# Optimization experiments

Measured on AMD Instinct MI355X. Metric: run time of the kernel, lower is better.

The kernel has to match this reference:

```python
import jax, jax.numpy as jnp
import numpy as np

N = 100000   # nodes
E = 1600000  # edges
G = 64       # graphs
D_IN, D_H, D_OUT = 128, 128, 64


def setup_inputs() -> dict:
    key = jax.random.key(0)
    ks = jax.random.split(key, 24)
    def p(k, shape, fan_in):
        return jax.random.normal(k, shape, jnp.float32) / np.sqrt(fan_in)
    inp = {
        "x": jax.random.normal(ks[0], (N, D_IN), jnp.float32),
        "W0r": p(ks[1], (D_H, D_IN), D_IN), "W0i": p(ks[2], (D_H, D_IN), D_IN),
        "b0r": jnp.zeros((D_H,), jnp.float32), "b0i": jnp.zeros((D_H,), jnp.float32),
        "M0r": p(ks[3], (D_H, D_H), D_H), "M0i": p(ks[4], (D_H, D_H), D_H),
        "c0r": jnp.zeros((D_H,), jnp.float32), "c0i": jnp.zeros((D_H,), jnp.float32),
        "t0r": jnp.float32(1.0), "t0i": jnp.zeros((1,), jnp.float32),
        "W1r": p(ks[5], (D_OUT, D_H), D_H), "W1i": p(ks[6], (D_OUT, D_H), D_H),
        "b1r": jnp.zeros((D_OUT,), jnp.float32), "b1i": jnp.zeros((D_OUT,), jnp.float32),
        "M1r": p(ks[7], (D_OUT, D_OUT), D_OUT), "M1i": p(ks[8], (D_OUT, D_OUT), D_OUT),
        "c1r": jnp.zeros((D_OUT,), jnp.float32), "c1i": jnp.zeros((D_OUT,), jnp.float32),
        "t1r": jnp.float32(1.0), "t1i": jnp.zeros((1,), jnp.float32),
        "edge_index": jax.random.randint(ks[9], (2, E), 0, N, dtype=jnp.int64),
        "batch": jnp.sort(jax.random.randint(ks[10], (N,), 0, G, dtype=jnp.int64)),
    }
    return inp


def _complex_relu(z):
    return jax.nn.relu(z.real) + 1j * jax.nn.relu(z.imag)


def _layer(x, Wr, Wi, br, bi, Mr, Mi, cr, ci, tr, ti, src, dst):
    # complex linear: x @ W^T + b
    W = Wr + 1j * Wi
    x = x @ W.T + (br + 1j * bi)
    x = _complex_relu(x)
    t = tr + 1j * ti  # complex time param, shape [1]
    time_factor = jnp.exp(-1j * t)
    # msg_lin applied at node level (linear commutes with gather), then gather at src
    m = (x @ (Mr + 1j * Mi).T + (cr + 1j * ci)) * time_factor
    aggr = jax.ops.segment_sum(m[src], dst, num_segments=N)
    ef = jnp.exp(-1j * t * 0.5)
    return x * ef + aggr * (1 - ef)


def reference(x, W0r, W0i, b0r, b0i, M0r, M0i, c0r, c0i, t0r, t0i,
              W1r, W1i, b1r, b1i, M1r, M1i, c1r, c1i, t1r, t1i,
              edge_index, batch):
    src, dst = edge_index[0], edge_index[1]
    xc = x.astype(jnp.complex64)
    xc = _layer(xc, W0r, W0i, b0r, b0i, M0r, M0i, c0r, c0i, t0r, t0i, src, dst)
    xc = _layer(xc, W1r, W1i, b1r, b1i, M1r, M1i, c1r, c1i, t1r, t1i, src, dst)
    a = jnp.abs(xc)  # [N, D_OUT] float32
    sums = jax.ops.segment_sum(a, batch, num_segments=G)
    counts = jax.ops.segment_sum(jnp.ones((N,), a.dtype), batch, num_segments=G)
    mean = sums / jnp.clip(counts, 1.0)[:, None]
    return jax.nn.log_softmax(mean, axis=1)
```

## Files before the change

### kernel.cpp

```cpp
#include <hip/hip_runtime.h>

typedef __attribute__((ext_vector_type(8))) short bf16x8;
typedef __attribute__((ext_vector_type(4))) float f32x4;

__device__ __forceinline__ float b2f(unsigned short u) {
    return __uint_as_float(((unsigned int)u) << 16);
}
__device__ __forceinline__ unsigned short f2b(float f) {
    unsigned int u = __float_as_uint(f);
    unsigned int r = (u + 0x7FFFu + ((u >> 16) & 1u)) >> 16;
    return (unsigned short)r;
}

#define EDGE_CHUNK 2048

__global__ __launch_bounds__(256) void prep_build_kernel(
    const float* __restrict__ W0r, const float* __restrict__ W0i, unsigned short* __restrict__ V0,
    const float* __restrict__ M0r, const float* __restrict__ M0i, unsigned short* __restrict__ VM0,
    const float* __restrict__ W1r, const float* __restrict__ W1i, unsigned short* __restrict__ V1,
    const float* __restrict__ M1r, const float* __restrict__ M1i, unsigned short* __restrict__ VM1,
    const int* __restrict__ src, const int* __restrict__ dst,
    int* __restrict__ deg, int* __restrict__ csr, int E, int N)
{
    int b = blockIdx.x;
    if (b < 64) {
        int idx = b * 256 + threadIdx.x;
        int j = idx >> 7, k = idx & 127;
        V0[(size_t)(2 * j) * 128 + k]     = f2b(W0r[idx]);
        V0[(size_t)(2 * j + 1) * 128 + k] = f2b(W0i[idx]);
    } else if (b < 128) {
        int idx = (b - 64) * 256 + threadIdx.x;
        int j = idx >> 7, kk = idx & 127;
        float wr = M0r[idx], wi = M0i[idx];
        unsigned short* r0 = VM0 + (size_t)(2 * j) * 256 + 2 * kk;
        unsigned short* r1 = VM0 + (size_t)(2 * j + 1) * 256 + 2 * kk;
        r0[0] = f2b(wr);  r0[1] = f2b(-wi);
        r1[0] = f2b(wi);  r1[1] = f2b(wr);
    } else if (b < 160) {
        int idx = (b - 128) * 256 + threadIdx.x;
        int j = idx >> 7, kk = idx & 127;
        float wr = W1r[idx], wi = W1i[idx];
        unsigned short* r0 = V1 + (size_t)(2 * j) * 256 + 2 * kk;
        unsigned short* r1 = V1 + (size_t)(2 * j + 1) * 256 + 2 * kk;
        r0[0] = f2b(wr);  r0[1] = f2b(-wi);
        r1[0] = f2b(wi);  r1[1] = f2b(wr);
    } else if (b < 176) {
        int idx = (b - 160) * 256 + threadIdx.x;
        int j = idx >> 6, kk = idx & 63;
        float wr = M1r[idx], wi = M1i[idx];
        unsigned short* r0 = VM1 + (size_t)(2 * j) * 128 + 2 * kk;
        unsigned short* r1 = VM1 + (size_t)(2 * j + 1) * 128 + 2 * kk;
        r0[0] = f2b(wr);  r0[1] = f2b(-wi);
        r1[0] = f2b(wi);  r1[1] = f2b(wr);
    } else {
        int vb = b - 176;
        int x  = vb & 7;
        int c  = vb >> 3;
        int lo = (int)((long long)N * x / 8);
        int hi = (int)((long long)N * (x + 1) / 8);
        int base = c * EDGE_CHUNK;
        int end  = min(base + EDGE_CHUNK, E);
        for (int e = base + threadIdx.x; e < end; e += 256) {
            int d = __builtin_nontemporal_load(dst + e);
            if (d >= lo && d < hi) {
                int s = __builtin_nontemporal_load(src + e);
                if ((unsigned)s < (unsigned)N) {
                    int pos = atomicAdd(&deg[d], 1);
                    if (pos < 64) csr[((size_t)d << 6) + pos] = s;
                }
            }
        }
    }
}

template<int Kr, int TWOJ, int AMODE, bool CRELU, bool MIX, bool WF8>
__global__ __launch_bounds__(256) void mfma_cgemm_kernel(
    const void* __restrict__ Xv,
    const unsigned short* __restrict__ Vg,
    const float* __restrict__ br, const float* __restrict__ bi,
    const float* __restrict__ trp, const float* __restrict__ tip,
    const unsigned short* __restrict__ Hin, const int* __restrict__ degp,
    unsigned short* __restrict__ Out, unsigned char* __restrict__ Of8,
    int nNodes)
{
    constexpr int TILES  = TWOJ / 16;
    constexpr int FT     = TILES / 4;
    constexpr int CHUNKS = Kr / 32;
    constexpr int VROW   = 40;
    static_assert(TILES % 4 == 0, "TILES % 4");

    __shared__ __align__(16) unsigned short sV[TWOJ * VROW];
    __shared__ __align__(16) unsigned short sA[64 * VROW];

    const int tid  = threadIdx.x;
    const int w    = tid >> 6;
    const int lane = tid & 63;
    const int l15  = lane & 15;
    const int q    = lane >> 4;
    const int n0   = blockIdx.x * 64;
    const int tq   = w * FT;

    f32x4 acc[FT][4];
    #pragma unroll
    for (int t = 0; t < FT; ++t)
        #pragma unroll
        for (int nt = 0; nt < 4; ++nt) acc[t][nt] = (f32x4){0.f, 0.f, 0.f, 0.f};

    for (int kc = 0; kc < CHUNKS; ++kc) {
        #pragma unroll
        for (int it = 0; it < TWOJ / 64; ++it) {
            int idx = it * 256 + tid;
            int row = idx >> 2;
            int seg = idx & 3;
            *(uint4*)(sV + row * VROW + seg * 8) =
                *(const uint4*)(Vg + (size_t)row * Kr + kc * 32 + seg * 8);
        }
        if constexpr (AMODE == 0) {
            const float* X = (const float*)Xv;
            #pragma unroll
            for (int it = 0; it < 2; ++it) {
                int idx = it * 256 + tid;
                int nl = idx >> 3;
                int cg = idx & 7;
                int n  = n0 + nl;
                f32x4 v = (f32x4){0.f, 0.f, 0.f, 0.f};
                if (n < nNodes)
                    v = __builtin_nontemporal_load(
                        (const f32x4*)(X + (size_t)n * Kr + kc * 32 + cg * 4));
                *(ushort4*)(sA + nl * VROW + cg * 4) =
                    make_ushort4(f2b(v[0]), f2b(v[1]), f2b(v[2]), f2b(v[3]));
            }
        } else {
            const unsigned short* X = (const unsigned short*)Xv;
            int nl  = tid >> 2;
            int seg = tid & 3;
            int n   = n0 + nl;
            uint4 v = make_uint4(0, 0, 0, 0);
            if (n < nNodes)
                v = *(const uint4*)(X + (size_t)n * Kr + kc * 32 + seg * 8);
            *(uint4*)(sA + nl * VROW + seg * 8) = v;
        }
        __syncthreads();

        bf16x8 bfrag[4];
        #pragma unroll
        for (int nt = 0; nt < 4; ++nt)
            bfrag[nt] = *(const bf16x8*)(sA + (nt * 16 + l15) * VROW + q * 8);
        #pragma unroll
        for (int t = 0; t < FT; ++t) {
            bf16x8 afrag = *(const bf16x8*)(sV + ((tq + t) * 16 + l15) * VROW + q * 8);
            #pragma unroll
            for (int nt = 0; nt < 4; ++nt)
                acc[t][nt] = __builtin_amdgcn_mfma_f32_16x16x32_bf16(
                    afrag, bfrag[nt], acc[t][nt], 0, 0, 0);
        }
        __syncthreads();
    }

    float Fr = 1.f, Fi = 0.f, efr = 1.f, efi = 0.f;
    if constexpr (MIX) {
        float tr = trp[0], ti = tip[0];
        float er  = expf(ti);
        float tfr =  er * cosf(tr);
        float tfi = -er * sinf(tr);
        float eh  = expf(0.5f * ti);
        efr =  eh * cosf(0.5f * tr);
        efi = -eh * sinf(0.5f * tr);
        float omr = 1.f - efr, omi = -efi;
        Fr = tfr * omr - tfi * omi;
        Fi = tfr * omi + tfi * omr;
    }
    #pragma unroll
    for (int nt = 0; nt < 4; ++nt) {
        int n = n0 + nt * 16 + l15;
        if (n >= nNodes) continue;
        float dg = 0.f;
        if constexpr (MIX) dg = (float)degp[n];
        #pragma unroll
        for (int t = 0; t < FT; ++t) {
            int f0 = (tq + t) * 16 + q * 4;
            int j0 = f0 >> 1;
            float re0, im0, re1, im1;
            if constexpr (MIX) {
                float ar0 = acc[t][nt][0] + dg * br[j0];
                float ai0 = acc[t][nt][1] + dg * bi[j0];
                float ar1 = acc[t][nt][2] + dg * br[j0 + 1];
                float ai1 = acc[t][nt][3] + dg * bi[j0 + 1];
                re0 = ar0 * Fr - ai0 * Fi;  im0 = ar0 * Fi + ai0 * Fr;
                re1 = ar1 * Fr - ai1 * Fi;  im1 = ar1 * Fi + ai1 * Fr;
                ushort4 hu = *(const ushort4*)(Hin + (size_t)n * TWOJ + f0);
                float hr0 = b2f(hu.x), hi0 = b2f(hu.y), hr1 = b2f(hu.z), hi1 = b2f(hu.w);
                re0 += hr0 * efr - hi0 * efi;  im0 += hr0 * efi + hi0 * efr;
                re1 += hr1 * efr - hi1 * efi;  im1 += hr1 * efi + hi1 * efr;
            } else {
                re0 = acc[t][nt][0] + br[j0];
                im0 = acc[t][nt][1] + bi[j0];
                re1 = acc[t][nt][2] + br[j0 + 1];
                im1 = acc[t][nt][3] + bi[j0 + 1];
                if constexpr (CRELU) {
                    re0 = fmaxf(re0, 0.f); im0 = fmaxf(im0, 0.f);
                    re1 = fmaxf(re1, 0.f); im1 = fmaxf(im1, 0.f);
                }
            }
            *(ushort4*)(Out + (size_t)n * TWOJ + f0) =
                make_ushort4(f2b(re0), f2b(im0), f2b(re1), f2b(im1));
            if constexpr (WF8) {
                int pk = 0;
                pk = __builtin_amdgcn_cvt_pk_fp8_f32(re0, im0, pk, false);
                pk = __builtin_amdgcn_cvt_pk_fp8_f32(re1, im1, pk, true);
                *(int*)(Of8 + (size_t)n * TWOJ + f0) = pk;
            }
        }
    }
}

template<int ROWE>
__global__ __launch_bounds__(256) void gather_f8_kernel(
    const unsigned char* __restrict__ h8, unsigned short* __restrict__ agg,
    const int* __restrict__ deg, const int* __restrict__ csr, int N)
{
    constexpr int LPR = ROWE / 16;
    constexpr int NPW = 64 / LPR;
    const int tid  = threadIdx.x;
    const int lane = tid & 63;
    const int wid  = (blockIdx.x * 256 + tid) >> 6;
    if (wid * NPW >= N) return;
    const int g    = lane / LPR;
    const int sub  = lane % LPR;
    const int nid  = wid * NPW + g;
    const bool nv  = nid < N;
    int dg = 0;
    if (nv) dg = min(deg[nid], 64);

    uint4 cq0 = make_uint4(0, 0, 0, 0), cq1 = make_uint4(0, 0, 0, 0);
    if (nv) {
        const uint4* cp = (const uint4*)csr + ((size_t)nid << 4);
        cq0 = cp[sub];
        if constexpr (LPR == 8) cq1 = cp[8 + sub];
    }

    int mx = dg;
    mx = max(mx, __shfl_xor(mx, 32, 64));
    mx = max(mx, __shfl_xor(mx, 16, 64));
    if constexpr (LPR == 8) mx = max(mx, __shfl_xor(mx, 8, 64));

    float a[16];
    #pragma unroll
    for (int k = 0; k < 16; ++k) a[k] = 0.f;

    const unsigned char* hp = h8 + sub * 16;
    const int gb = g * LPR;

    #define CVT16(uu)                                                          \
        {                                                                      \
            auto p0 = __builtin_amdgcn_cvt_pk_f32_fp8((uu).x, false);          \
            a[0] += p0[0];   a[1] += p0[1];                                    \
            auto p1 = __builtin_amdgcn_cvt_pk_f32_fp8((uu).x, true);           \
            a[2] += p1[0];   a[3] += p1[1];                                    \
            auto p2 = __builtin_amdgcn_cvt_pk_f32_fp8((uu).y, false);          \
            a[4] += p2[0];   a[5] += p2[1];                                    \
            auto p3 = __builtin_amdgcn_cvt_pk_f32_fp8((uu).y, true);           \
            a[6] += p3[0];   a[7] += p3[1];                                    \
            auto p4 = __builtin_amdgcn_cvt_pk_f32_fp8((uu).z, false);          \
            a[8] += p4[0];   a[9] += p4[1];                                    \
            auto p5 = __builtin_amdgcn_cvt_pk_f32_fp8((uu).z, true);           \
            a[10] += p5[0];  a[11] += p5[1];                                   \
            auto p6 = __builtin_amdgcn_cvt_pk_f32_fp8((uu).w, false);          \
            a[12] += p6[0];  a[13] += p6[1];                                   \
            auto p7 = __builtin_amdgcn_cvt_pk_f32_fp8((uu).w, true);           \
            a[14] += p7[0];  a[15] += p7[1];                                   \
        }

    for (int e = 0; e < mx; e += 8) {
        uint4 cq = cq0;
        if constexpr (LPR == 8) { if (e & 32) cq = cq1; }
        const int o0 = gb + ((e & (4 * LPR - 1)) >> 2);
        const int o1 = o0 + 1;
        int s0 = __shfl((int)cq.x, o0, 64);
        int s1 = __shfl((int)cq.y, o0, 64);
        int s2 = __shfl((int)cq.z, o0, 64);
        int s3 = __shfl((int)cq.w, o0, 64);
        int s4 = __shfl((int)cq.x, o1, 64);
        int s5 = __shfl((int)cq.y, o1, 64);
        int s6 = __shfl((int)cq.z, o1, 64);
        int s7 = __shfl((int)cq.w, o1, 64);
        uint4 u0 = make_uint4(0,0,0,0), u1 = make_uint4(0,0,0,0);
        uint4 u2 = make_uint4(0,0,0,0), u3 = make_uint4(0,0,0,0);
        uint4 u4 = make_uint4(0,0,0,0), u5 = make_uint4(0,0,0,0);
        uint4 u6 = make_uint4(0,0,0,0), u7 = make_uint4(0,0,0,0);
        if (e + 0 < dg) u0 = *(const uint4*)(hp + (size_t)(unsigned)s0 * ROWE);
        if (e + 1 < dg) u1 = *(const uint4*)(hp + (size_t)(unsigned)s1 * ROWE);
        if (e + 2 < dg) u2 = *(const uint4*)(hp + (size_t)(unsigned)s2 * ROWE);
        if (e + 3 < dg) u3 = *(const uint4*)(hp + (size_t)(unsigned)s3 * ROWE);
        if (e + 4 < dg) u4 = *(const uint4*)(hp + (size_t)(unsigned)s4 * ROWE);
        if (e + 5 < dg) u5 = *(const uint4*)(hp + (size_t)(unsigned)s5 * ROWE);
        if (e + 6 < dg) u6 = *(const uint4*)(hp + (size_t)(unsigned)s6 * ROWE);
        if (e + 7 < dg) u7 = *(const uint4*)(hp + (size_t)(unsigned)s7 * ROWE);
        CVT16(u0) CVT16(u1) CVT16(u2) CVT16(u3)
        CVT16(u4) CVT16(u5) CVT16(u6) CVT16(u7)
    }
    #undef CVT16

    if (nv) {
        unsigned short* op = agg + (size_t)nid * ROWE + sub * 16;
        *(ushort4*)(op)      = make_ushort4(f2b(a[0]),  f2b(a[1]),  f2b(a[2]),  f2b(a[3]));
        *(ushort4*)(op + 4)  = make_ushort4(f2b(a[4]),  f2b(a[5]),  f2b(a[6]),  f2b(a[7]));
        *(ushort4*)(op + 8)  = make_ushort4(f2b(a[8]),  f2b(a[9]),  f2b(a[10]), f2b(a[11]));
        *(ushort4*)(op + 12) = make_ushort4(f2b(a[12]), f2b(a[13]), f2b(a[14]), f2b(a[15]));
    }
}

__global__ __launch_bounds__(256) void abs_reduce_kernel(
    const unsigned short* __restrict__ z, const int* __restrict__ batch,
    float* __restrict__ sums, int N)
{
    constexpr int NPW = 16;
    int wid  = (blockIdx.x * 256 + threadIdx.x) >> 6;
    int lane = threadIdx.x & 63;
    int nBeg = wid * NPW;
    if (nBeg >= N) return;
    int nEnd = min(nBeg + NPW, N);

    float acc = 0.f;
    int cur_g = batch[nBeg];
    for (int n = nBeg; n < nEnd; ++n) {
        unsigned int u = *(const unsigned int*)(z + ((size_t)n << 7) + (lane << 1));
        float zr = b2f((unsigned short)(u & 0xffffu));
        float zi = b2f((unsigned short)(u >> 16));
        float a = sqrtf(zr * zr + zi * zi);
        int g = batch[n];
        if (g != cur_g) {
            if ((unsigned)cur_g < 64u) unsafeAtomicAdd(&sums[cur_g * 64 + lane], acc);
            acc = 0.f;
            cur_g = g;
        }
        acc += a;
    }
    if ((unsigned)cur_g < 64u) unsafeAtomicAdd(&sums[cur_g * 64 + lane], acc);
}

__global__ __launch_bounds__(64) void finalize_kernel(
    const float* __restrict__ sums, const int* __restrict__ batch,
    float* __restrict__ out, int N)
{
    int g = blockIdx.x, d = threadIdx.x;
    __shared__ int cnt_s;
    if (d == 0) {
        int lo = 0, hi = N;
        while (lo < hi) { int mid = (lo + hi) >> 1; if (batch[mid] < g) lo = mid + 1; else hi = mid; }
        int lo2 = lo, hi2 = N;
        while (lo2 < hi2) { int mid = (lo2 + hi2) >> 1; if (batch[mid] < g + 1) lo2 = mid + 1; else hi2 = mid; }
        cnt_s = lo2 - lo;
    }
    __syncthreads();
    float c = fmaxf((float)cnt_s, 1.0f);
    float m = sums[g * 64 + d] / c;
    float mx = m;
    #pragma unroll
    for (int o = 32; o > 0; o >>= 1) mx = fmaxf(mx, __shfl_xor(mx, o, 64));
    float e = expf(m - mx);
    float s = e;
    #pragma unroll
    for (int o = 32; o > 0; o >>= 1) s += __shfl_xor(s, o, 64);
    out[g * 64 + d] = m - mx - logf(s);
}

extern "C" void kernel_launch(void* const* d_in, const int* in_sizes, int n_in,
                              void* d_out, int out_size, void* d_ws, size_t ws_size,
                              hipStream_t stream)
{
    const float* x   = (const float*)d_in[0];
    const float* W0r = (const float*)d_in[1];
    const float* W0i = (const float*)d_in[2];
    const float* b0r = (const float*)d_in[3];
    const float* b0i = (const float*)d_in[4];
    const float* M0r = (const float*)d_in[5];
    const float* M0i = (const float*)d_in[6];
    const float* c0r = (const float*)d_in[7];
    const float* c0i = (const float*)d_in[8];
    const float* t0r = (const float*)d_in[9];
    const float* t0i = (const float*)d_in[10];
    const float* W1r = (const float*)d_in[11];
    const float* W1i = (const float*)d_in[12];
    const float* b1r = (const float*)d_in[13];
    const float* b1i = (const float*)d_in[14];
    const float* M1r = (const float*)d_in[15];
    const float* M1i = (const float*)d_in[16];
    const float* c1r = (const float*)d_in[17];
    const float* c1i = (const float*)d_in[18];
    const float* t1r = (const float*)d_in[19];
    const float* t1i = (const float*)d_in[20];
    const int* edge  = (const int*)d_in[21];
    const int* batch = (const int*)d_in[22];

    const int N = in_sizes[0] / 128;
    const int E = in_sizes[21] / 2;
    const int* src = edge;
    const int* dst = edge + E;

    unsigned short* h0   = (unsigned short*)d_ws;
    unsigned short* aggA = h0 + (size_t)N * 256;
    unsigned short* h1   = aggA + (size_t)N * 256;
    unsigned short* aggB = h1 + (size_t)N * 128;
    int*   deg  = (int*)(aggB + (size_t)N * 128);
    int*   csr  = deg + N;
    float* sums = (float*)(csr + (size_t)N * 64);
    unsigned short* V0  = (unsigned short*)(sums + 4096);
    unsigned short* VM0 = V0  + 256 * 128;
    unsigned short* V1  = VM0 + 256 * 256;
    unsigned short* VM1 = V1  + 128 * 256;
    unsigned char* hf8 = (unsigned char*)(VM1 + 128 * 128);

    const int gemmGrid  = (N + 63) / 64;
    const int buildGrid = ((E + EDGE_CHUNK - 1) / EDGE_CHUNK) * 8;
    const int pbGrid    = 176 + buildGrid;
    const int g256Grid  = (N + 15) / 16;
    const int g128Grid  = (N + 31) / 32;
    const int wave16Grid = ((N + 15) / 16 * 64 + 255) / 256;

    hipMemsetAsync(deg, 0, N * sizeof(int), stream);
    hipMemsetAsync(sums, 0, 4096 * sizeof(float), stream);
    prep_build_kernel<<<pbGrid, 256, 0, stream>>>(
        W0r, W0i, V0, M0r, M0i, VM0, W1r, W1i, V1, M1r, M1i, VM1,
        src, dst, deg, csr, E, N);

    mfma_cgemm_kernel<128,256,0,true,false,true><<<gemmGrid, 256, 0, stream>>>(
        x, V0, b0r, b0i, nullptr, nullptr, nullptr, nullptr, h0, hf8, N);
    gather_f8_kernel<256><<<g256Grid, 256, 0, stream>>>(hf8, aggA, deg, csr, N);
    mfma_cgemm_kernel<256,256,1,false,true,false><<<gemmGrid, 256, 0, stream>>>(
        aggA, VM0, c0r, c0i, t0r, t0i, h0, deg, h0, nullptr, N);

    mfma_cgemm_kernel<256,128,1,true,false,true><<<gemmGrid, 256, 0, stream>>>(
        h0, V1, b1r, b1i, nullptr, nullptr, nullptr, nullptr, h1, hf8, N);
    gather_f8_kernel<128><<<g128Grid, 256, 0, stream>>>(hf8, aggB, deg, csr, N);
    mfma_cgemm_kernel<128,128,1,false,true,false><<<gemmGrid, 256, 0, stream>>>(
        aggB, VM1, c1r, c1i, t1r, t1i, h1, deg, h1, nullptr, N);

    abs_reduce_kernel<<<wave16Grid, 256, 0, stream>>>(h1, batch, sums, N);
    finalize_kernel<<<64, 64, 0, stream>>>(sums, batch, (float*)d_out, N);
}
```

Measured before the change: 492.5 us.

## Fuse layer-0 message GEMM epilogue with layer-1 input GEMM in one kernel

```diff
diff --git a/kernel.cpp b/kernel.cpp
--- a/kernel.cpp
+++ b/kernel.cpp
@@ -214,6 +214,162 @@
     }
 }
 
+__global__ __launch_bounds__(256) void mfma_dual_kernel(
+    const unsigned short* __restrict__ Xagg,
+    const unsigned short* __restrict__ VM,
+    const unsigned short* __restrict__ Vg2,
+    const float* __restrict__ cr, const float* __restrict__ ci,
+    const float* __restrict__ trp, const float* __restrict__ tip,
+    const float* __restrict__ b1r, const float* __restrict__ b1i,
+    const unsigned short* __restrict__ Hin,
+    const int* __restrict__ degp,
+    unsigned short* __restrict__ Out,
+    unsigned char* __restrict__ Of8,
+    int nNodes)
+{
+    constexpr int VROW = 40;
+    __shared__ __align__(16) unsigned short sV[256 * VROW];
+    __shared__ __align__(16) unsigned short sA[64 * VROW];
+    __shared__ __align__(16) unsigned short x1b[8 * 64 * VROW];
+
+    const int tid  = threadIdx.x;
+    const int w    = tid >> 6;
+    const int lane = tid & 63;
+    const int l15  = lane & 15;
+    const int q    = lane >> 4;
+    const int n0   = blockIdx.x * 64;
+
+    {
+        f32x4 acc[4][4];
+        #pragma unroll
+        for (int t = 0; t < 4; ++t)
+            #pragma unroll
+            for (int nt = 0; nt < 4; ++nt) acc[t][nt] = (f32x4){0.f, 0.f, 0.f, 0.f};
+
+        for (int kc = 0; kc < 8; ++kc) {
+            #pragma unroll
+            for (int it = 0; it < 4; ++it) {
+                int idx = it * 256 + tid;
+                int row = idx >> 2;
+                int seg = idx & 3;
+                *(uint4*)(sV + row * VROW + seg * 8) =
+                    *(const uint4*)(VM + (size_t)row * 256 + kc * 32 + seg * 8);
+            }
+            {
+                int nl  = tid >> 2;
+                int seg = tid & 3;
+                int n   = n0 + nl;
+                uint4 v = make_uint4(0, 0, 0, 0);
+                if (n < nNodes)
+                    v = *(const uint4*)(Xagg + (size_t)n * 256 + kc * 32 + seg * 8);
+                *(uint4*)(sA + nl * VROW + seg * 8) = v;
+            }
+            __syncthreads();
+            bf16x8 bfrag[4];
+            #pragma unroll
+            for (int nt = 0; nt < 4; ++nt)
+                bfrag[nt] = *(const bf16x8*)(sA + (nt * 16 + l15) * VROW + q * 8);
+            #pragma unroll
+            for (int t = 0; t < 4; ++t) {
+                bf16x8 afrag = *(const bf16x8*)(sV + ((w * 4 + t) * 16 + l15) * VROW + q * 8);
+                #pragma unroll
+                for (int nt = 0; nt < 4; ++nt)
+                    acc[t][nt] = __builtin_amdgcn_mfma_f32_16x16x32_bf16(
+                        afrag, bfrag[nt], acc[t][nt], 0, 0, 0);
+            }
+            __syncthreads();
+        }
+
+        float tr = trp[0], ti = tip[0];
+        float er  = expf(ti);
+        float tfr =  er * cosf(tr);
+        float tfi = -er * sinf(tr);
+        float eh  = expf(0.5f * ti);
+        float efr =  eh * cosf(0.5f * tr);
+        float efi = -eh * sinf(0.5f * tr);
+        float omr = 1.f - efr, omi = -efi;
+        float Fr = tfr * omr - tfi * omi;
+        float Fi = tfr * omi + tfi * omr;
+
+        #pragma unroll
+        for (int nt = 0; nt < 4; ++nt) {
+            int n = n0 + nt * 16 + l15;
+            if (n >= nNodes) continue;
+            float dg = (float)degp[n];
+            #pragma unroll
+            for (int t = 0; t < 4; ++t) {
+                int f0 = (w * 4 + t) * 16 + q * 4;
+                int j0 = f0 >> 1;
+                float ar0 = acc[t][nt][0] + dg * cr[j0];
+                float ai0 = acc[t][nt][1] + dg * ci[j0];
+                float ar1 = acc[t][nt][2] + dg * cr[j0 + 1];
+                float ai1 = acc[t][nt][3] + dg * ci[j0 + 1];
+                float re0 = ar0 * Fr - ai0 * Fi, im0 = ar0 * Fi + ai0 * Fr;
+                float re1 = ar1 * Fr - ai1 * Fi, im1 = ar1 * Fi + ai1 * Fr;
+                ushort4 hu = *(const ushort4*)(Hin + (size_t)n * 256 + f0);
+                float hr0 = b2f(hu.x), hi0 = b2f(hu.y), hr1 = b2f(hu.z), hi1 = b2f(hu.w);
+                re0 += hr0 * efr - hi0 * efi;  im0 += hr0 * efi + hi0 * efr;
+                re1 += hr1 * efr - hi1 * efi;  im1 += hr1 * efi + hi1 * efr;
+                *(ushort4*)(x1b + ((f0 >> 5) * 64 + nt * 16 + l15) * VROW + (f0 & 31)) =
+                    make_ushort4(f2b(re0), f2b(im0), f2b(re1), f2b(im1));
+            }
+        }
+    }
+    __syncthreads();
+
+    f32x4 acc2[2][4];
+    #pragma unroll
+    for (int t = 0; t < 2; ++t)
+        #pragma unroll
+        for (int nt = 0; nt < 4; ++nt) acc2[t][nt] = (f32x4){0.f, 0.f, 0.f, 0.f};
+
+    for (int kc = 0; kc < 8; ++kc) {
+        #pragma unroll
+        for (int it = 0; it < 2; ++it) {
+            int idx = it * 256 + tid;
+            int row = idx >> 2;
+            int seg = idx & 3;
+            *(uint4*)(sV + row * VROW + seg * 8) =
+                *(const uint4*)(Vg2 + (size_t)row * 256 + kc * 32 + seg * 8);
+        }
+        __syncthreads();
+        bf16x8 bfrag[4];
+        #pragma unroll
+        for (int nt = 0; nt < 4; ++nt)
+            bfrag[nt] = *(const bf16x8*)(x1b + ((size_t)(kc * 64 + nt * 16 + l15)) * VROW + q * 8);
+        #pragma unroll
+        for (int t = 0; t < 2; ++t) {
+            bf16x8 afrag = *(const bf16x8*)(sV + ((w * 2 + t) * 16 + l15) * VROW + q * 8);
+            #pragma unroll
+            for (int nt = 0; nt < 4; ++nt)
+                acc2[t][nt] = __builtin_amdgcn_mfma_f32_16x16x32_bf16(
+                    afrag, bfrag[nt], acc2[t][nt], 0, 0, 0);
+        }
+        __syncthreads();
+    }
+
+    #pragma unroll
+    for (int nt = 0; nt < 4; ++nt) {
+        int n = n0 + nt * 16 + l15;
+        if (n >= nNodes) continue;
+        #pragma unroll
+        for (int t = 0; t < 2; ++t) {
+            int f0 = (w * 2 + t) * 16 + q * 4;
+            int j0 = f0 >> 1;
+            float re0 = fmaxf(acc2[t][nt][0] + b1r[j0], 0.f);
+            float im0 = fmaxf(acc2[t][nt][1] + b1i[j0], 0.f);
+            float re1 = fmaxf(acc2[t][nt][2] + b1r[j0 + 1], 0.f);
+            float im1 = fmaxf(acc2[t][nt][3] + b1i[j0 + 1], 0.f);
+            *(ushort4*)(Out + (size_t)n * 128 + f0) =
+                make_ushort4(f2b(re0), f2b(im0), f2b(re1), f2b(im1));
+            int pk = 0;
+            pk = __builtin_amdgcn_cvt_pk_fp8_f32(re0, im0, pk, false);
+            pk = __builtin_amdgcn_cvt_pk_fp8_f32(re1, im1, pk, true);
+            *(int*)(Of8 + (size_t)n * 128 + f0) = pk;
+        }
+    }
+}
+
 template<int ROWE>
 __global__ __launch_bounds__(256) void gather_f8_kernel(
     const unsigned char* __restrict__ h8, unsigned short* __restrict__ agg,
@@ -427,11 +583,10 @@
     mfma_cgemm_kernel<128,256,0,true,false,true><<<gemmGrid, 256, 0, stream>>>(
         x, V0, b0r, b0i, nullptr, nullptr, nullptr, nullptr, h0, hf8, N);
     gather_f8_kernel<256><<<g256Grid, 256, 0, stream>>>(hf8, aggA, deg, csr, N);
-    mfma_cgemm_kernel<256,256,1,false,true,false><<<gemmGrid, 256, 0, stream>>>(
-        aggA, VM0, c0r, c0i, t0r, t0i, h0, deg, h0, nullptr, N);
-
-    mfma_cgemm_kernel<256,128,1,true,false,true><<<gemmGrid, 256, 0, stream>>>(
-        h0, V1, b1r, b1i, nullptr, nullptr, nullptr, nullptr, h1, hf8, N);
+
+    mfma_dual_kernel<<<gemmGrid, 256, 0, stream>>>(
+        aggA, VM0, V1, c0r, c0i, t0r, t0i, b1r, b1i, h0, deg, h1, hf8, N);
+
     gather_f8_kernel<128><<<g128Grid, 256, 0, stream>>>(hf8, aggB, deg, csr, N);
     mfma_cgemm_kernel<128,128,1,false,true,false><<<gemmGrid, 256, 0, stream>>>(
         aggB, VM1, c1r, c1i, t1r, t1i, h1, deg, h1, nullptr, N);
```

New measurement: 476.4 us. 1.03x faster.
